# Performance work log

Hardware: AMD Instinct MI355X
Metric: run time of the kernel (lower is better)

## Reference

```python
import jax, jax.numpy as jnp
import numpy as np

N_NODES = 20000


def _gcn_norm(edge_index, n):
    src, dst = edge_index[0], edge_index[1]
    # degree of A + I (self-loops), all edge weights 1
    deg = jax.ops.segment_sum(jnp.ones(src.shape[0], jnp.float32), dst, num_segments=n) + 1.0
    dinv = jax.lax.rsqrt(deg)
    norm = dinv[src] * dinv[dst]          # [E]
    self_norm = dinv * dinv               # [N] self-loop coefficient = 1/deg
    return src, dst, norm, self_norm


def _gcn_layer(x, W, b, src, dst, norm, self_norm):
    # x: [B, N, Fin]; W: [Fin, Fout]
    h = jnp.einsum('bnf,fo->bno', x, W)   # transform first (PyG GCNConv order)
    msg = h[:, src, :] * norm[None, :, None]                      # [B, E, Fout]
    agg = jax.vmap(lambda m: jax.ops.segment_sum(m, dst, num_segments=x.shape[1]))(msg)
    agg = agg + h * self_norm[None, :, None]                      # self-loop term
    return agg + b


def setup_inputs() -> dict:
    key = jax.random.key(0)
    ks = jax.random.split(key, 8)
    B, N, Fin, H, O, E = 2, N_NODES, 256, 256, 64, 320000
    s = lambda f: 1.0 / np.sqrt(f)
    return {
        'x': jax.random.normal(ks[0], (B, N, Fin), jnp.float32),
        'W1': jax.random.normal(ks[1], (Fin, H), jnp.float32) * s(Fin),
        'b1': jnp.zeros((H,), jnp.float32),
        'W2': jax.random.normal(ks[2], (H, H), jnp.float32) * s(H),
        'b2': jnp.zeros((H,), jnp.float32),
        'Wfc': jax.random.normal(ks[3], (H, O), jnp.float32) * s(H),
        'bfc': jnp.zeros((O,), jnp.float32),
        'edge_index': jax.random.randint(ks[4], (2, E), 0, N, jnp.int64),
    }


def reference(x, W1, b1, W2, b2, Wfc, bfc, edge_index):
    src, dst, norm, self_norm = _gcn_norm(edge_index, x.shape[1])
    h = jax.nn.relu(_gcn_layer(x, W1, b1, src, dst, norm, self_norm))
    h = jax.nn.relu(_gcn_layer(h, W2, b2, src, dst, norm, self_norm))
    pooled = jnp.mean(h, axis=1)          # mean over nodes -> [B, H]
    return pooled @ Wfc + bfc             # [B, O]
```

## Files before the change

### kernel.cpp

```cpp
#include <hip/hip_runtime.h>

#define NNODES 20000
#define BATCH  2
#define FEAT   256
#define OOUT   64
#define PBLK   200
#define MROWS  (BATCH * NNODES)
#define MPAD   40192

typedef short  bhalf8 __attribute__((ext_vector_type(8)));
typedef float  floatx4 __attribute__((ext_vector_type(4)));
typedef float  floatx2 __attribute__((ext_vector_type(2)));

__device__ __forceinline__ float bf2f(unsigned short u) {
  return __uint_as_float(((unsigned int)u) << 16);
}
__device__ __forceinline__ unsigned short f2bf(float f) {
  unsigned int u = __float_as_uint(f);
  return (unsigned short)((u + 0x7fffu + ((u >> 16) & 1u)) >> 16);
}

__device__ __forceinline__ unsigned int pack4_fp8(float a, float b, float c, float d) {
  int p = __builtin_amdgcn_cvt_pk_fp8_f32(a, b, 0, false);
  p = __builtin_amdgcn_cvt_pk_fp8_f32(c, d, p, true);
  return (unsigned int)p;
}

__global__ __launch_bounds__(256) void detect_zero_kernel(const int* __restrict__ raw,
                                                          int* __restrict__ flag,
                                                          int* __restrict__ cnt,
                                                          int* __restrict__ fill, int E) {
  for (int i = threadIdx.x; i < NNODES; i += 256) { cnt[i] = 0; fill[i] = 0; }
  __shared__ int any;
  if (threadIdx.x == 0) any = 0;
  __syncthreads();
  int nchk = E < 2048 ? E : 2048;
  for (int i = threadIdx.x; i < nchk; i += blockDim.x)
    if (raw[2 * i + 1] != 0) any = 1;
  __syncthreads();
  if (threadIdx.x == 0) *flag = any;
}

__global__ void convert_count_kernel(const int* __restrict__ raw, const int* __restrict__ flag,
                                     int* __restrict__ s32, int* __restrict__ d32,
                                     int* __restrict__ cnt, int E) {
  int e = blockIdx.x * blockDim.x + threadIdx.x;
  if (e >= E) return;
  int s, d;
  if (*flag) { s = raw[e];     d = raw[E + e]; }
  else       { s = raw[2 * e]; d = raw[2 * (E + e)]; }
  s32[e] = s; d32[e] = d;
  atomicAdd(&cnt[d], 1);
}

__global__ __launch_bounds__(1024) void scan_dinv_kernel(const int* __restrict__ cnt,
                                                         int* __restrict__ row_start,
                                                         float* __restrict__ dinv, int n) {
  __shared__ int wsum[16];
  __shared__ int carry_s;
  int tid = threadIdx.x, lane = tid & 63, wv = tid >> 6;
  if (tid == 0) carry_s = 0;
  __syncthreads();
  for (int base = 0; base < n; base += 1024) {
    int v = (base + tid < n) ? cnt[base + tid] : 0;
    if (base + tid < n) dinv[base + tid] = 1.0f / sqrtf((float)(v + 1));
    int x = v;
#pragma unroll
    for (int off = 1; off < 64; off <<= 1) {
      int t = __shfl_up(x, off);
      if (lane >= off) x += t;
    }
    if (lane == 63) wsum[wv] = x;
    __syncthreads();
    int carry = carry_s;
    if (wv == 0) {
      int s = (lane < 16) ? wsum[lane] : 0;
#pragma unroll
      for (int off = 1; off < 16; off <<= 1) {
        int t = __shfl_up(s, off);
        if (lane >= off) s += t;
      }
      if (lane < 16) wsum[lane] = s;
    }
    __syncthreads();
    int woff = wv ? wsum[wv - 1] : 0;
    int total = wsum[15];
    if (base + tid < n) row_start[base + tid] = carry + woff + x - v;
    __syncthreads();
    if (tid == 0) carry_s = carry + total;
  }
  if (tid == 0) row_start[n] = carry_s;
}

__global__ void scatter_kernel(const int* __restrict__ s32, const int* __restrict__ d32,
                               const int* __restrict__ row_start, int* __restrict__ fill,
                               const float* __restrict__ dinv,
                               int* __restrict__ csr_src, float* __restrict__ csr_norm, int E) {
  int e = blockIdx.x * blockDim.x + threadIdx.x;
  if (e >= E) return;
  int s = s32[e], d = d32[e];
  int p = row_start[d] + atomicAdd(&fill[d], 1);
  csr_src[p] = s;
  csr_norm[p] = dinv[s] * dinv[d];
}

__global__ __launch_bounds__(256) void wprep_kernel(const float* __restrict__ W1,
                                                    const float* __restrict__ W2,
                                                    unsigned short* __restrict__ W1hi,
                                                    unsigned short* __restrict__ W1lo,
                                                    unsigned short* __restrict__ W2hi,
                                                    unsigned short* __restrict__ W2lo) {
  int which = blockIdx.x >> 8;
  int idx = (blockIdx.x & 255) * 256 + threadIdx.x;
  const float* W = which ? W2 : W1;
  unsigned short* Whi = which ? W2hi : W1hi;
  unsigned short* Wlo = which ? W2lo : W1lo;
  int k = idx >> 8, n = idx & 255;
  float w = W[idx];
  unsigned short hi = f2bf(w);
  unsigned short lo = f2bf(w - bf2f(hi));
  int g = n >> 4, ln = n & 15;
  int ks = k >> 5, ch = (k >> 3) & 3, j = k & 7;
  int addr = ((ks * 16 + g) * 64 + ch * 16 + ln) * 8 + j;
  Whi[addr] = hi;
  Wlo[addr] = lo;
}

template <int AFP32>
__global__ __launch_bounds__(256) void gemm_mfma(const void* __restrict__ Av,
                                                 const unsigned short* __restrict__ Whi,
                                                 const unsigned short* __restrict__ Wlo,
                                                 unsigned int* __restrict__ C) {
  __shared__ unsigned short lds[2][8192];
  int tid = threadIdx.x, lane = tid & 63, wv = tid >> 6;
  int half = blockIdx.y;
  int bm = blockIdx.x * 128;
  int kc = (lane >> 4) * 8;

  const float* Af          = (const float*)Av;
  const unsigned short* Ab = (const unsigned short*)Av;

  int mr[2];
#pragma unroll
  for (int t = 0; t < 2; ++t) {
    int m = bm + wv * 32 + t * 16 + (lane & 15);
    mr[t] = m >= MROWS ? MROWS - 1 : m;
  }

  floatx4 acc[2][8];
#pragma unroll
  for (int t = 0; t < 2; ++t)
#pragma unroll
    for (int g = 0; g < 8; ++g) acc[t][g] = (floatx4)(0.0f);

  bhalf8 st[4];

  auto stage_load = [&](int ks) {
#pragma unroll
    for (int i2 = 0; i2 < 4; ++i2) {
      int u = i2 * 256 + tid;
      int hl = u >> 9, g = (u >> 6) & 7, l = u & 63;
      const unsigned short* Wp = hl ? Wlo : Whi;
      st[i2] = *(const bhalf8*)&Wp[((size_t)(ks * 16 + half * 8 + g) * 64 + l) * 8];
    }
  };
  auto stage_write = [&](int buf) {
#pragma unroll
    for (int i2 = 0; i2 < 4; ++i2) {
      int u = i2 * 256 + tid;
      *(bhalf8*)&lds[buf][(size_t)u * 8] = st[i2];
    }
  };
  auto load_a = [&](int ks, bhalf8 (&a)[2]) {
#pragma unroll
    for (int t = 0; t < 2; ++t) {
      if (AFP32) {
        const float* p = &Af[(size_t)mr[t] * FEAT + ks * 32 + kc];
        float4 u = *(const float4*)p;
        float4 v = *(const float4*)(p + 4);
        a[t][0] = (short)f2bf(u.x); a[t][1] = (short)f2bf(u.y);
        a[t][2] = (short)f2bf(u.z); a[t][3] = (short)f2bf(u.w);
        a[t][4] = (short)f2bf(v.x); a[t][5] = (short)f2bf(v.y);
        a[t][6] = (short)f2bf(v.z); a[t][7] = (short)f2bf(v.w);
      } else {
        a[t] = *(const bhalf8*)&Ab[(size_t)mr[t] * FEAT + ks * 32 + kc];
      }
    }
  };
  auto step = [&](int buf, bhalf8 (&a)[2]) {
#pragma unroll
    for (int g = 0; g < 8; ++g) {
      bhalf8 bh = *(const bhalf8*)&lds[buf][((size_t)g * 64 + lane) * 8];
      bhalf8 bl = *(const bhalf8*)&lds[buf][((size_t)(512 + g * 64) + lane) * 8];
#pragma unroll
      for (int t = 0; t < 2; ++t)
        acc[t][g] = __builtin_amdgcn_mfma_f32_16x16x32_bf16(bh, a[t], acc[t][g], 0, 0, 0);
#pragma unroll
      for (int t = 0; t < 2; ++t)
        acc[t][g] = __builtin_amdgcn_mfma_f32_16x16x32_bf16(bl, a[t], acc[t][g], 0, 0, 0);
    }
  };

  stage_load(0);
  stage_write(0);
  __syncthreads();
  bhalf8 aC[2];
  load_a(0, aC);
  int cur = 0;
#pragma unroll
  for (int ks = 0; ks < 8; ++ks) {
    bhalf8 aN[2];
    if (ks < 7) {
      stage_load(ks + 1);
      load_a(ks + 1, aN);
    }
    step(cur, aC);
    if (ks < 7) {
      stage_write(cur ^ 1);
      __syncthreads();
      aC[0] = aN[0]; aC[1] = aN[1];
    }
    cur ^= 1;
  }

  int nc = (lane >> 4) * 4;
#pragma unroll
  for (int t = 0; t < 2; ++t) {
    int om = bm + wv * 32 + t * 16 + (lane & 15);
#pragma unroll
    for (int g = 0; g < 8; ++g) {
      int col = (half * 8 + g) * 16 + nc;
      C[(size_t)om * 64 + (col >> 2)] =
          pack4_fp8(acc[t][g][0], acc[t][g][1], acc[t][g][2], acc[t][g][3]);
    }
  }
}

__global__ __launch_bounds__(128) void agg_kernel(const uint4* __restrict__ h8,
                                                  const int* __restrict__ row_start,
                                                  const int* __restrict__ csr_src,
                                                  const float* __restrict__ csr_norm,
                                                  const float* __restrict__ dinv,
                                                  const float* __restrict__ bias,
                                                  unsigned short* __restrict__ out) {
  int n = blockIdx.x;
  int b = threadIdx.x >> 6;
  int lane = threadIdx.x & 63;
  int q = lane >> 4;
  int cl = lane & 15;
  const uint4* hb = h8 + (size_t)b * NNODES * 16;

  float a[16];
#pragma unroll
  for (int j = 0; j < 16; ++j) a[j] = 0.0f;

  auto dec_fma = [&](uint4 m, float w) {
    unsigned int mm[4] = {m.x, m.y, m.z, m.w};
#pragma unroll
    for (int j = 0; j < 4; ++j) {
      floatx2 lo = __builtin_amdgcn_cvt_pk_f32_fp8((int)mm[j], false);
      floatx2 hi = __builtin_amdgcn_cvt_pk_f32_fp8((int)mm[j], true);
      a[j * 4 + 0] = fmaf(w, lo[0], a[j * 4 + 0]);
      a[j * 4 + 1] = fmaf(w, lo[1], a[j * 4 + 1]);
      a[j * 4 + 2] = fmaf(w, hi[0], a[j * 4 + 2]);
      a[j * 4 + 3] = fmaf(w, hi[1], a[j * 4 + 3]);
    }
  };

  float di = dinv[n];
  if (q == 0) dec_fma(hb[(size_t)n * 16 + cl], di * di);

  int s0 = row_start[n], s1 = row_start[n + 1];
  int i = s0 + q;
  for (; i + 4 < s1; i += 8) {
    int sa = csr_src[i], sb = csr_src[i + 4];
    float wa = csr_norm[i], wb = csr_norm[i + 4];
    uint4 ma = hb[(size_t)sa * 16 + cl];
    uint4 mb = hb[(size_t)sb * 16 + cl];
    dec_fma(ma, wa);
    dec_fma(mb, wb);
  }
  if (i < s1) dec_fma(hb[(size_t)csr_src[i] * 16 + cl], csr_norm[i]);

#pragma unroll
  for (int j = 0; j < 16; ++j) {
    a[j] += __shfl_xor(a[j], 16);
    a[j] += __shfl_xor(a[j], 32);
  }

  if (q == 0) {
    int c = cl * 16;
    unsigned short o[16];
#pragma unroll
    for (int j = 0; j < 16; ++j)
      o[j] = f2bf(fmaxf(a[j] + bias[c + j], 0.0f));
    unsigned short* dst = &out[((size_t)b * NNODES + n) * FEAT + c];
    *(uint4*)dst = *(uint4*)&o[0];
    *(uint4*)(dst + 8) = *(uint4*)&o[8];
  }
}

__global__ __launch_bounds__(256) void pool_partial(const unsigned short* __restrict__ h2,
                                                    float* __restrict__ partials) {
  int blk = blockIdx.x;
  int c = threadIdx.x;
  int chunk = NNODES / PBLK;
  int n0 = blk * chunk;
  float s0 = 0.f, s1 = 0.f;
  for (int n = n0; n < n0 + chunk; ++n) {
    s0 += bf2f(h2[((size_t)0 * NNODES + n) * FEAT + c]);
    s1 += bf2f(h2[((size_t)1 * NNODES + n) * FEAT + c]);
  }
  partials[(blk * 2 + 0) * FEAT + c] = s0;
  partials[(blk * 2 + 1) * FEAT + c] = s1;
}

__global__ __launch_bounds__(256) void pool_fc(const float* __restrict__ partials,
                                               const float* __restrict__ Wfc, const float* __restrict__ bfc,
                                               float* __restrict__ out) {
  __shared__ float pooled[BATCH][FEAT];
  int t = threadIdx.x;
  float s0 = 0.f, s1 = 0.f;
  for (int p = 0; p < PBLK; ++p) {
    s0 += partials[(p * 2 + 0) * FEAT + t];
    s1 += partials[(p * 2 + 1) * FEAT + t];
  }
  pooled[0][t] = s0 / (float)NNODES;
  pooled[1][t] = s1 / (float)NNODES;
  __syncthreads();
  if (t < BATCH * OOUT) {
    int b = t >> 6, o = t & 63;
    float acc = bfc[o];
    for (int c2 = 0; c2 < FEAT; ++c2)
      acc = fmaf(pooled[b][c2], Wfc[c2 * OOUT + o], acc);
    out[b * OOUT + o] = acc;
  }
}

extern "C" void kernel_launch(void* const* d_in, const int* in_sizes, int n_in,
                              void* d_out, int out_size, void* d_ws, size_t ws_size,
                              hipStream_t stream) {
  const float* x    = (const float*)d_in[0];
  const float* W1   = (const float*)d_in[1];
  const float* b1   = (const float*)d_in[2];
  const float* W2   = (const float*)d_in[3];
  const float* b2   = (const float*)d_in[4];
  const float* Wfc  = (const float*)d_in[5];
  const float* bfc  = (const float*)d_in[6];
  const int*   eraw = (const int*)d_in[7];
  int E = in_sizes[7] / 2;
  float* out = (float*)d_out;

  char* ws = (char*)d_ws;
  size_t off = 0;
  auto alloc = [&](size_t elems) -> void* {
    void* p = ws + off * 4;
    off += (elems + 3) & ~(size_t)3;
    return p;
  };
  int*   flag      = (int*)alloc(4);
  int*   s32       = (int*)alloc(E);
  int*   d32      = (int*)alloc(E);
  int*   cnt       = (int*)alloc(NNODES);
  float* dinv      = (float*)alloc(NNODES);
  int*   row_start = (int*)alloc(NNODES + 1);
  int*   fill      = (int*)alloc(NNODES);
  int*   csr_src   = (int*)alloc(E);
  float* csr_norm  = (float*)alloc(E);
  unsigned short* w1hi = (unsigned short*)alloc(65536 / 2);
  unsigned short* w1lo = (unsigned short*)alloc(65536 / 2);
  unsigned short* w2hi = (unsigned short*)alloc(65536 / 2);
  unsigned short* w2lo = (unsigned short*)alloc(65536 / 2);
  unsigned int*   h8   = (unsigned int*)alloc((size_t)MPAD * 64);
  unsigned short* a1   = (unsigned short*)alloc((size_t)MROWS * FEAT / 2);
  float* partials  = (float*)alloc((size_t)PBLK * BATCH * FEAT);

  int eg = (E + 255) / 256;
  detect_zero_kernel<<<1, 256, 0, stream>>>(eraw, flag, cnt, fill, E);
  convert_count_kernel<<<eg, 256, 0, stream>>>(eraw, flag, s32, d32, cnt, E);
  scan_dinv_kernel<<<1, 1024, 0, stream>>>(cnt, row_start, dinv, NNODES);
  scatter_kernel<<<eg, 256, 0, stream>>>(s32, d32, row_start, fill, dinv, csr_src, csr_norm, E);
  wprep_kernel<<<512, 256, 0, stream>>>(W1, W2, w1hi, w1lo, w2hi, w2lo);

  dim3 ggrid(MPAD / 128, 2);
  gemm_mfma<1><<<ggrid, 256, 0, stream>>>(x, w1hi, w1lo, h8);
  agg_kernel<<<NNODES, 128, 0, stream>>>((const uint4*)h8, row_start, csr_src, csr_norm, dinv, b1, a1);
  gemm_mfma<0><<<ggrid, 256, 0, stream>>>(a1, w2hi, w2lo, h8);
  agg_kernel<<<NNODES, 128, 0, stream>>>((const uint4*)h8, row_start, csr_src, csr_norm, dinv, b2, a1);
  pool_partial<<<PBLK, 256, 0, stream>>>(a1, partials);
  pool_fc<<<1, 256, 0, stream>>>(partials, Wfc, bfc, out);
}
```

Before: 203.0 us.

## Fuse all GCN stages into one cooperative persistent megakernel with grid syncs

Replaces the chain of separate launches (CSR build, weight prep, two GEMMs, two aggregations, pooling, FC) with a single cooperative kernel that walks through the stages using grid-wide barriers. It also fuses the second aggregation with mean-pooling so the second-layer activations are never written out, and parallelizes the degree scan across blocks. The goal is to remove launch gaps and one full activation round trip, at the cost of grid-sync overhead, a fixed persistent grid that may underfill some stages, and register pressure from the merged code.

Measured after the change: 695.7 us. +242.7%, slower.

```diff
diff --git a/kernel.cpp b/kernel.cpp
--- a/kernel.cpp
+++ b/kernel.cpp
@@ -1,12 +1,16 @@
 #include <hip/hip_runtime.h>
+#include <hip/hip_cooperative_groups.h>
+
+namespace cg = cooperative_groups;
 
 #define NNODES 20000
 #define BATCH  2
 #define FEAT   256
 #define OOUT   64
-#define PBLK   200
-#define MROWS  (BATCH * NNODES)
+#define MROWS  40000
 #define MPAD   40192
+#define NTILES 628
+#define NCHUNK 20
 
 typedef short  bhalf8 __attribute__((ext_vector_type(8)));
 typedef float  floatx4 __attribute__((ext_vector_type(4)));
@@ -19,124 +23,29 @@
   unsigned int u = __float_as_uint(f);
   return (unsigned short)((u + 0x7fffu + ((u >> 16) & 1u)) >> 16);
 }
-
 __device__ __forceinline__ unsigned int pack4_fp8(float a, float b, float c, float d) {
   int p = __builtin_amdgcn_cvt_pk_fp8_f32(a, b, 0, false);
   p = __builtin_amdgcn_cvt_pk_fp8_f32(c, d, p, true);
   return (unsigned int)p;
 }
 
-__global__ __launch_bounds__(256) void detect_zero_kernel(const int* __restrict__ raw,
-                                                          int* __restrict__ flag,
-                                                          int* __restrict__ cnt,
-                                                          int* __restrict__ fill, int E) {
-  for (int i = threadIdx.x; i < NNODES; i += 256) { cnt[i] = 0; fill[i] = 0; }
-  __shared__ int any;
-  if (threadIdx.x == 0) any = 0;
-  __syncthreads();
-  int nchk = E < 2048 ? E : 2048;
-  for (int i = threadIdx.x; i < nchk; i += blockDim.x)
-    if (raw[2 * i + 1] != 0) any = 1;
-  __syncthreads();
-  if (threadIdx.x == 0) *flag = any;
-}
-
-__global__ void convert_count_kernel(const int* __restrict__ raw, const int* __restrict__ flag,
-                                     int* __restrict__ s32, int* __restrict__ d32,
-                                     int* __restrict__ cnt, int E) {
-  int e = blockIdx.x * blockDim.x + threadIdx.x;
-  if (e >= E) return;
-  int s, d;
-  if (*flag) { s = raw[e];     d = raw[E + e]; }
-  else       { s = raw[2 * e]; d = raw[2 * (E + e)]; }
-  s32[e] = s; d32[e] = d;
-  atomicAdd(&cnt[d], 1);
-}
-
-__global__ __launch_bounds__(1024) void scan_dinv_kernel(const int* __restrict__ cnt,
-                                                         int* __restrict__ row_start,
-                                                         float* __restrict__ dinv, int n) {
-  __shared__ int wsum[16];
-  __shared__ int carry_s;
+struct GArgs {
+  const float *x, *W1, *b1, *W2, *b2, *Wfc, *bfc;
+  const int* eraw;
+  int E;
+  int *flag, *s32, *d32, *cnt, *row_start, *fill, *csr_src, *chunkAux;
+  float *dinv, *csr_norm, *partials, *out;
+  unsigned short *w1hi, *w1lo, *w2hi, *w2lo, *a1;
+  unsigned int* h8;
+};
+
+template <int AFP32>
+__device__ __forceinline__ void gemm_tile(const void* Av, const unsigned short* Whi,
+                                          const unsigned short* Wlo, unsigned int* C,
+                                          int bx, int half, unsigned short* ldsb) {
   int tid = threadIdx.x, lane = tid & 63, wv = tid >> 6;
-  if (tid == 0) carry_s = 0;
-  __syncthreads();
-  for (int base = 0; base < n; base += 1024) {
-    int v = (base + tid < n) ? cnt[base + tid] : 0;
-    if (base + tid < n) dinv[base + tid] = 1.0f / sqrtf((float)(v + 1));
-    int x = v;
-#pragma unroll
-    for (int off = 1; off < 64; off <<= 1) {
-      int t = __shfl_up(x, off);
-      if (lane >= off) x += t;
-    }
-    if (lane == 63) wsum[wv] = x;
-    __syncthreads();
-    int carry = carry_s;
-    if (wv == 0) {
-      int s = (lane < 16) ? wsum[lane] : 0;
-#pragma unroll
-      for (int off = 1; off < 16; off <<= 1) {
-        int t = __shfl_up(s, off);
-        if (lane >= off) s += t;
-      }
-      if (lane < 16) wsum[lane] = s;
-    }
-    __syncthreads();
-    int woff = wv ? wsum[wv - 1] : 0;
-    int total = wsum[15];
-    if (base + tid < n) row_start[base + tid] = carry + woff + x - v;
-    __syncthreads();
-    if (tid == 0) carry_s = carry + total;
-  }
-  if (tid == 0) row_start[n] = carry_s;
-}
-
-__global__ void scatter_kernel(const int* __restrict__ s32, const int* __restrict__ d32,
-                               const int* __restrict__ row_start, int* __restrict__ fill,
-                               const float* __restrict__ dinv,
-                               int* __restrict__ csr_src, float* __restrict__ csr_norm, int E) {
-  int e = blockIdx.x * blockDim.x + threadIdx.x;
-  if (e >= E) return;
-  int s = s32[e], d = d32[e];
-  int p = row_start[d] + atomicAdd(&fill[d], 1);
-  csr_src[p] = s;
-  csr_norm[p] = dinv[s] * dinv[d];
-}
-
-__global__ __launch_bounds__(256) void wprep_kernel(const float* __restrict__ W1,
-                                                    const float* __restrict__ W2,
-                                                    unsigned short* __restrict__ W1hi,
-                                                    unsigned short* __restrict__ W1lo,
-                                                    unsigned short* __restrict__ W2hi,
-                                                    unsigned short* __restrict__ W2lo) {
-  int which = blockIdx.x >> 8;
-  int idx = (blockIdx.x & 255) * 256 + threadIdx.x;
-  const float* W = which ? W2 : W1;
-  unsigned short* Whi = which ? W2hi : W1hi;
-  unsigned short* Wlo = which ? W2lo : W1lo;
-  int k = idx >> 8, n = idx & 255;
-  float w = W[idx];
-  unsigned short hi = f2bf(w);
-  unsigned short lo = f2bf(w - bf2f(hi));
-  int g = n >> 4, ln = n & 15;
-  int ks = k >> 5, ch = (k >> 3) & 3, j = k & 7;
-  int addr = ((ks * 16 + g) * 64 + ch * 16 + ln) * 8 + j;
-  Whi[addr] = hi;
-  Wlo[addr] = lo;
-}
-
-template <int AFP32>
-__global__ __launch_bounds__(256) void gemm_mfma(const void* __restrict__ Av,
-                                                 const unsigned short* __restrict__ Whi,
-                                                 const unsigned short* __restrict__ Wlo,
-                                                 unsigned int* __restrict__ C) {
-  __shared__ unsigned short lds[2][8192];
-  int tid = threadIdx.x, lane = tid & 63, wv = tid >> 6;
-  int half = blockIdx.y;
-  int bm = blockIdx.x * 128;
+  int bm = bx * 128;
   int kc = (lane >> 4) * 8;
-
   const float* Af          = (const float*)Av;
   const unsigned short* Ab = (const unsigned short*)Av;
 
@@ -146,7 +55,6 @@
     int m = bm + wv * 32 + t * 16 + (lane & 15);
     mr[t] = m >= MROWS ? MROWS - 1 : m;
   }
-
   floatx4 acc[2][8];
 #pragma unroll
   for (int t = 0; t < 2; ++t)
@@ -154,7 +62,6 @@
     for (int g = 0; g < 8; ++g) acc[t][g] = (floatx4)(0.0f);
 
   bhalf8 st[4];
-
   auto stage_load = [&](int ks) {
 #pragma unroll
     for (int i2 = 0; i2 < 4; ++i2) {
@@ -168,7 +75,7 @@
 #pragma unroll
     for (int i2 = 0; i2 < 4; ++i2) {
       int u = i2 * 256 + tid;
-      *(bhalf8*)&lds[buf][(size_t)u * 8] = st[i2];
+      *(bhalf8*)&ldsb[(size_t)buf * 8192 + (size_t)u * 8] = st[i2];
     }
   };
   auto load_a = [&](int ks, bhalf8 (&a)[2]) {
@@ -190,8 +97,8 @@
   auto step = [&](int buf, bhalf8 (&a)[2]) {
 #pragma unroll
     for (int g = 0; g < 8; ++g) {
-      bhalf8 bh = *(const bhalf8*)&lds[buf][((size_t)g * 64 + lane) * 8];
-      bhalf8 bl = *(const bhalf8*)&lds[buf][((size_t)(512 + g * 64) + lane) * 8];
+      bhalf8 bh = *(const bhalf8*)&ldsb[(size_t)buf * 8192 + ((size_t)g * 64 + lane) * 8];
+      bhalf8 bl = *(const bhalf8*)&ldsb[(size_t)buf * 8192 + ((size_t)(512 + g * 64) + lane) * 8];
 #pragma unroll
       for (int t = 0; t < 2; ++t)
         acc[t][g] = __builtin_amdgcn_mfma_f32_16x16x32_bf16(bh, a[t], acc[t][g], 0, 0, 0);
@@ -236,19 +143,14 @@
   }
 }
 
-__global__ __launch_bounds__(128) void agg_kernel(const uint4* __restrict__ h8,
-                                                  const int* __restrict__ row_start,
-                                                  const int* __restrict__ csr_src,
-                                                  const float* __restrict__ csr_norm,
-                                                  const float* __restrict__ dinv,
-                                                  const float* __restrict__ bias,
-                                                  unsigned short* __restrict__ out) {
-  int n = blockIdx.x;
-  int b = threadIdx.x >> 6;
-  int lane = threadIdx.x & 63;
+template <int WRITE>
+__device__ __forceinline__ void agg_node(const GArgs& g, int n, int tid2,
+                                         const float* bias, float* pacc) {
+  int b = tid2 >> 6;
+  int lane = tid2 & 63;
   int q = lane >> 4;
   int cl = lane & 15;
-  const uint4* hb = h8 + (size_t)b * NNODES * 16;
+  const uint4* hb = (const uint4*)g.h8 + (size_t)b * NNODES * 16;
 
   float a[16];
 #pragma unroll
@@ -267,20 +169,20 @@
     }
   };
 
-  float di = dinv[n];
+  float di = g.dinv[n];
   if (q == 0) dec_fma(hb[(size_t)n * 16 + cl], di * di);
 
-  int s0 = row_start[n], s1 = row_start[n + 1];
+  int s0 = g.row_start[n], s1 = g.row_start[n + 1];
   int i = s0 + q;
   for (; i + 4 < s1; i += 8) {
-    int sa = csr_src[i], sb = csr_src[i + 4];
-    float wa = csr_norm[i], wb = csr_norm[i + 4];
+    int sa = g.csr_src[i], sb = g.csr_src[i + 4];
+    float wa = g.csr_norm[i], wb = g.csr_norm[i + 4];
     uint4 ma = hb[(size_t)sa * 16 + cl];
     uint4 mb = hb[(size_t)sb * 16 + cl];
     dec_fma(ma, wa);
     dec_fma(mb, wb);
   }
-  if (i < s1) dec_fma(hb[(size_t)csr_src[i] * 16 + cl], csr_norm[i]);
+  if (i < s1) dec_fma(hb[(size_t)g.csr_src[i] * 16 + cl], g.csr_norm[i]);
 
 #pragma unroll
   for (int j = 0; j < 16; ++j) {
@@ -288,105 +190,220 @@
     a[j] += __shfl_xor(a[j], 32);
   }
 
-  if (q == 0) {
-    int c = cl * 16;
-    unsigned short o[16];
-#pragma unroll
-    for (int j = 0; j < 16; ++j)
-      o[j] = f2bf(fmaxf(a[j] + bias[c + j], 0.0f));
-    unsigned short* dst = &out[((size_t)b * NNODES + n) * FEAT + c];
-    *(uint4*)dst = *(uint4*)&o[0];
-    *(uint4*)(dst + 8) = *(uint4*)&o[8];
-  }
-}
-
-__global__ __launch_bounds__(256) void pool_partial(const unsigned short* __restrict__ h2,
-                                                    float* __restrict__ partials) {
-  int blk = blockIdx.x;
-  int c = threadIdx.x;
-  int chunk = NNODES / PBLK;
-  int n0 = blk * chunk;
-  float s0 = 0.f, s1 = 0.f;
-  for (int n = n0; n < n0 + chunk; ++n) {
-    s0 += bf2f(h2[((size_t)0 * NNODES + n) * FEAT + c]);
-    s1 += bf2f(h2[((size_t)1 * NNODES + n) * FEAT + c]);
-  }
-  partials[(blk * 2 + 0) * FEAT + c] = s0;
-  partials[(blk * 2 + 1) * FEAT + c] = s1;
-}
-
-__global__ __launch_bounds__(256) void pool_fc(const float* __restrict__ partials,
-                                               const float* __restrict__ Wfc, const float* __restrict__ bfc,
-                                               float* __restrict__ out) {
-  __shared__ float pooled[BATCH][FEAT];
-  int t = threadIdx.x;
-  float s0 = 0.f, s1 = 0.f;
-  for (int p = 0; p < PBLK; ++p) {
-    s0 += partials[(p * 2 + 0) * FEAT + t];
-    s1 += partials[(p * 2 + 1) * FEAT + t];
-  }
-  pooled[0][t] = s0 / (float)NNODES;
-  pooled[1][t] = s1 / (float)NNODES;
-  __syncthreads();
-  if (t < BATCH * OOUT) {
-    int b = t >> 6, o = t & 63;
-    float acc = bfc[o];
-    for (int c2 = 0; c2 < FEAT; ++c2)
-      acc = fmaf(pooled[b][c2], Wfc[c2 * OOUT + o], acc);
-    out[b * OOUT + o] = acc;
+  if (WRITE) {
+    if (q == 0) {
+      int c = cl * 16;
+      unsigned short o[16];
+#pragma unroll
+      for (int j = 0; j < 16; ++j)
+        o[j] = f2bf(fmaxf(a[j] + bias[c + j], 0.0f));
+      unsigned short* dst = &g.a1[((size_t)b * NNODES + n) * FEAT + c];
+      *(uint4*)dst = *(uint4*)&o[0];
+      *(uint4*)(dst + 8) = *(uint4*)&o[8];
+    }
+  } else {
+    if (q == 0) {
+      int c = cl * 16;
+#pragma unroll
+      for (int j = 0; j < 16; ++j)
+        pacc[j] += fmaxf(a[j] + bias[c + j], 0.0f);
+    }
+  }
+}
+
+__global__ __launch_bounds__(256) void GCN_mega(GArgs g) {
+  cg::grid_group gg = cg::this_grid();
+  __shared__ __align__(16) char smem[32768];
+  const int tid = threadIdx.x, bid = blockIdx.x;
+  const int nblk = (int)gridDim.x;
+  const int nthr = nblk * 256;
+  const int gtid = bid * 256 + tid;
+
+  for (int i = gtid; i < NNODES; i += nthr) { g.cnt[i] = 0; g.fill[i] = 0; }
+  for (int idx = gtid; idx < 2 * FEAT * FEAT; idx += nthr) {
+    int which = idx >> 16, loc = idx & 65535;
+    const float* W = which ? g.W2 : g.W1;
+    unsigned short* Whi = which ? g.w2hi : g.w1hi;
+    unsigned short* Wlo = which ? g.w2lo : g.w1lo;
+    int k = loc >> 8, n = loc & 255;
+    float w = W[loc];
+    unsigned short hi = f2bf(w);
+    unsigned short lo = f2bf(w - bf2f(hi));
+    int gq = n >> 4, ln = n & 15;
+    int ks = k >> 5, ch = (k >> 3) & 3, j = k & 7;
+    int addr = ((ks * 16 + gq) * 64 + ch * 16 + ln) * 8 + j;
+    Whi[addr] = hi;
+    Wlo[addr] = lo;
+  }
+  if (bid == 0) {
+    int* any = (int*)smem;
+    if (tid == 0) *any = 0;
+    __syncthreads();
+    int nchk = g.E < 2048 ? g.E : 2048;
+    for (int i = tid; i < nchk; i += 256)
+      if (g.eraw[2 * i + 1] != 0) *any = 1;
+    __syncthreads();
+    if (tid == 0) *g.flag = *any;
+  }
+  gg.sync();
+
+  {
+    int isI32 = *g.flag;
+    for (int e = gtid; e < g.E; e += nthr) {
+      int s, d;
+      if (isI32) { s = g.eraw[e];     d = g.eraw[g.E + e]; }
+      else       { s = g.eraw[2 * e]; d = g.eraw[2 * (g.E + e)]; }
+      g.s32[e] = s; g.d32[e] = d;
+      atomicAdd(&g.cnt[d], 1);
+    }
+  }
+  gg.sync();
+
+  if (bid < NCHUNK) {
+    int base = bid * 1024 + tid * 4;
+    int v[4]; int tsum = 0;
+#pragma unroll
+    for (int j = 0; j < 4; ++j) { v[j] = (base + j < NNODES) ? g.cnt[base + j] : 0; tsum += v[j]; }
+    int lane = tid & 63, wv = tid >> 6;
+    int x = tsum;
+#pragma unroll
+    for (int off = 1; off < 64; off <<= 1) { int t = __shfl_up(x, off); if (lane >= off) x += t; }
+    int* wsum = (int*)smem;
+    if (lane == 63) wsum[wv] = x;
+    __syncthreads();
+    int woff = 0;
+    for (int w = 0; w < wv; ++w) woff += wsum[w];
+    int run = woff + x - tsum;
+#pragma unroll
+    for (int j = 0; j < 4; ++j) {
+      if (base + j < NNODES) {
+        g.row_start[base + j] = run;
+        g.dinv[base + j] = 1.0f / sqrtf((float)(v[j] + 1));
+      }
+      run += v[j];
+    }
+    if (tid == 0) g.chunkAux[bid] = wsum[0] + wsum[1] + wsum[2] + wsum[3];
+  }
+  gg.sync();
+
+  if (bid == 0 && tid == 0) {
+    int tot = 0;
+    for (int c = 0; c < NCHUNK; ++c) { int t = g.chunkAux[c]; g.chunkAux[c] = tot; tot += t; }
+    g.row_start[NNODES] = tot;
+  }
+  gg.sync();
+
+  for (int i = gtid; i < NNODES; i += nthr) g.row_start[i] += g.chunkAux[i >> 10];
+  gg.sync();
+
+  for (int e = gtid; e < g.E; e += nthr) {
+    int s = g.s32[e], d = g.d32[e];
+    int p = g.row_start[d] + atomicAdd(&g.fill[d], 1);
+    g.csr_src[p] = s;
+    g.csr_norm[p] = g.dinv[s] * g.dinv[d];
+  }
+  gg.sync();
+
+  for (int t = bid; t < NTILES; t += nblk)
+    gemm_tile<1>(g.x, g.w1hi, g.w1lo, g.h8, t >> 1, t & 1, (unsigned short*)smem);
+  gg.sync();
+
+  {
+    int nsub = tid >> 7, tid2 = tid & 127;
+    for (int n = bid * 2 + nsub; n < NNODES; n += nblk * 2)
+      agg_node<1>(g, n, tid2, g.b1, (float*)nullptr);
+  }
+  gg.sync();
+
+  for (int t = bid; t < NTILES; t += nblk)
+    gemm_tile<0>(g.a1, g.w2hi, g.w2lo, g.h8, t >> 1, t & 1, (unsigned short*)smem);
+  gg.sync();
+
+  {
+    float pacc[16];
+#pragma unroll
+    for (int j = 0; j < 16; ++j) pacc[j] = 0.0f;
+    int nsub = tid >> 7, tid2 = tid & 127;
+    for (int n = bid * 2 + nsub; n < NNODES; n += nblk * 2)
+      agg_node<0>(g, n, tid2, g.b2, pacc);
+
+    float* sp = (float*)smem;
+    for (int t2 = tid; t2 < 512; t2 += 256) sp[t2] = 0.0f;
+    __syncthreads();
+    int b = tid2 >> 6, lane = tid2 & 63, q = lane >> 4, cl = lane & 15;
+    if (q == 0) {
+#pragma unroll
+      for (int j = 0; j < 16; ++j)
+        atomicAdd(&sp[b * 256 + cl * 16 + j], pacc[j]);
+    }
+    __syncthreads();
+    for (int t2 = tid; t2 < 512; t2 += 256)
+      g.partials[(size_t)bid * 512 + t2] = sp[t2];
+  }
+  gg.sync();
+
+  if (bid < 2) {
+    float* pooled = (float*)smem;
+    float s = 0.0f;
+    for (int p = 0; p < nblk; ++p) s += g.partials[(size_t)p * 512 + bid * 256 + tid];
+    pooled[tid] = s / (float)NNODES;
+    __syncthreads();
+    if (tid < OOUT) {
+      float acc = g.bfc[tid];
+      for (int f = 0; f < FEAT; ++f)
+        acc = fmaf(pooled[f], g.Wfc[f * OOUT + tid], acc);
+      g.out[bid * OOUT + tid] = acc;
+    }
   }
 }
 
 extern "C" void kernel_launch(void* const* d_in, const int* in_sizes, int n_in,
                               void* d_out, int out_size, void* d_ws, size_t ws_size,
                               hipStream_t stream) {
-  const float* x    = (const float*)d_in[0];
-  const float* W1   = (const float*)d_in[1];
-  const float* b1   = (const float*)d_in[2];
-  const float* W2   = (const float*)d_in[3];
-  const float* b2   = (const float*)d_in[4];
-  const float* Wfc  = (const float*)d_in[5];
-  const float* bfc  = (const float*)d_in[6];
-  const int*   eraw = (const int*)d_in[7];
-  int E = in_sizes[7] / 2;
-  float* out = (float*)d_out;
+  GArgs a;
+  a.x    = (const float*)d_in[0];
+  a.W1   = (const float*)d_in[1];
+  a.b1   = (const float*)d_in[2];
+  a.W2   = (const float*)d_in[3];
+  a.b2   = (const float*)d_in[4];
+  a.Wfc  = (const float*)d_in[5];
+  a.bfc  = (const float*)d_in[6];
+  a.eraw = (const int*)d_in[7];
+  a.E    = in_sizes[7] / 2;
+  a.out  = (float*)d_out;
 
   char* ws = (char*)d_ws;
   size_t off = 0;
-  auto alloc = [&](size_t elems) -> void* {
+  auto alloc = [&](size_t elems4B) -> void* {
     void* p = ws + off * 4;
-    off += (elems + 3) & ~(size_t)3;
+    off += (elems4B + 3) & ~(size_t)3;
     return p;
   };
-  int*   flag      = (int*)alloc(4);
-  int*   s32       = (int*)alloc(E);
-  int*   d32      = (int*)alloc(E);
-  int*   cnt       = (int*)alloc(NNODES);
-  float* dinv      = (float*)alloc(NNODES);
-  int*   row_start = (int*)alloc(NNODES + 1);
-  int*   fill      = (int*)alloc(NNODES);
-  int*   csr_src   = (int*)alloc(E);
-  float* csr_norm  = (float*)alloc(E);
-  unsigned short* w1hi = (unsigned short*)alloc(65536 / 2);
-  unsigned short* w1lo = (unsigned short*)alloc(65536 / 2);
-  unsigned short* w2hi = (unsigned short*)alloc(65536 / 2);
-  unsigned short* w2lo = (unsigned short*)alloc(65536 / 2);
-  unsigned int*   h8   = (unsigned int*)alloc((size_t)MPAD * 64);
-  unsigned short* a1   = (unsigned short*)alloc((size_t)MROWS * FEAT / 2);
-  float* partials  = (float*)alloc((size_t)PBLK * BATCH * FEAT);
-
-  int eg = (E + 255) / 256;
-  detect_zero_kernel<<<1, 256, 0, stream>>>(eraw, flag, cnt, fill, E);
-  convert_count_kernel<<<eg, 256, 0, stream>>>(eraw, flag, s32, d32, cnt, E);
-  scan_dinv_kernel<<<1, 1024, 0, stream>>>(cnt, row_start, dinv, NNODES);
-  scatter_kernel<<<eg, 256, 0, stream>>>(s32, d32, row_start, fill, dinv, csr_src, csr_norm, E);
-  wprep_kernel<<<512, 256, 0, stream>>>(W1, W2, w1hi, w1lo, w2hi, w2lo);
-
-  dim3 ggrid(MPAD / 128, 2);
-  gemm_mfma<1><<<ggrid, 256, 0, stream>>>(x, w1hi, w1lo, h8);
-  agg_kernel<<<NNODES, 128, 0, stream>>>((const uint4*)h8, row_start, csr_src, csr_norm, dinv, b1, a1);
-  gemm_mfma<0><<<ggrid, 256, 0, stream>>>(a1, w2hi, w2lo, h8);
-  agg_kernel<<<NNODES, 128, 0, stream>>>((const uint4*)h8, row_start, csr_src, csr_norm, dinv, b2, a1);
-  pool_partial<<<PBLK, 256, 0, stream>>>(a1, partials);
-  pool_fc<<<1, 256, 0, stream>>>(partials, Wfc, bfc, out);
-}
+  int E = a.E;
+  a.flag      = (int*)alloc(4);
+  a.s32       = (int*)alloc(E);
+  a.d32       = (int*)alloc(E);
+  a.cnt       = (int*)alloc(NNODES);
+  a.dinv      = (float*)alloc(NNODES);
+  a.row_start = (int*)alloc(NNODES + 1);
+  a.fill      = (int*)alloc(NNODES);
+  a.csr_src   = (int*)alloc(E);
+  a.csr_norm  = (float*)alloc(E);
+  a.chunkAux  = (int*)alloc(32);
+  a.w1hi = (unsigned short*)alloc(65536 / 2);
+  a.w1lo = (unsigned short*)alloc(65536 / 2);
+  a.w2hi = (unsigned short*)alloc(65536 / 2);
+  a.w2lo = (unsigned short*)alloc(65536 / 2);
+  a.h8   = (unsigned int*)alloc((size_t)MPAD * 64);
+  a.a1   = (unsigned short*)alloc((size_t)MROWS * FEAT / 2);
+  a.partials = (float*)alloc((size_t)1024 * 512);
+
+  int nb = 0;
+  hipOccupancyMaxActiveBlocksPerMultiprocessor(&nb, GCN_mega, 256, 0);
+  if (nb < 1) nb = 1;
+  int grid = nb * 256;
+  if (grid > 1024) grid = 1024;
+
+  void* kp[1] = {&a};
+  hipLaunchCooperativeKernel(GCN_mega, dim3(grid), dim3(256), kp, 0, stream);
+}
```

## Interleave batch rows in fp8 features so one gather serves both batches

Applied to the files above, without the earlier changes.

The GEMM now writes the fp8 transformed features with the two batch copies of each node stored next to each other (row = node*2 + batch). Each neighbour gather in aggregation then fetches one contiguous 512-byte row covering both batches, instead of two separate 256-byte rows. The aggregation is re-split so each wave half handles different edges across all 32 column chunks, with an LDS step to combine the two waves. Weight prep, counter zeroing and the edge-format check are also merged into a single prep kernel to cut launches.

Result: faster. 188.9 us (-6.9%).

```diff
diff --git a/kernel.cpp b/kernel.cpp
--- a/kernel.cpp
+++ b/kernel.cpp
@@ -5,8 +5,9 @@
 #define FEAT   256
 #define OOUT   64
 #define PBLK   200
-#define MROWS  (BATCH * NNODES)
-#define MPAD   40192
+#define MROWS  40000
+#define NPB    20096
+#define H8ROWS 40192
 
 typedef short  bhalf8 __attribute__((ext_vector_type(8)));
 typedef float  floatx4 __attribute__((ext_vector_type(4)));
@@ -19,26 +20,48 @@
   unsigned int u = __float_as_uint(f);
   return (unsigned short)((u + 0x7fffu + ((u >> 16) & 1u)) >> 16);
 }
-
 __device__ __forceinline__ unsigned int pack4_fp8(float a, float b, float c, float d) {
   int p = __builtin_amdgcn_cvt_pk_fp8_f32(a, b, 0, false);
   p = __builtin_amdgcn_cvt_pk_fp8_f32(c, d, p, true);
   return (unsigned int)p;
 }
 
-__global__ __launch_bounds__(256) void detect_zero_kernel(const int* __restrict__ raw,
-                                                          int* __restrict__ flag,
-                                                          int* __restrict__ cnt,
-                                                          int* __restrict__ fill, int E) {
-  for (int i = threadIdx.x; i < NNODES; i += 256) { cnt[i] = 0; fill[i] = 0; }
-  __shared__ int any;
-  if (threadIdx.x == 0) any = 0;
-  __syncthreads();
-  int nchk = E < 2048 ? E : 2048;
-  for (int i = threadIdx.x; i < nchk; i += blockDim.x)
-    if (raw[2 * i + 1] != 0) any = 1;
-  __syncthreads();
-  if (threadIdx.x == 0) *flag = any;
+__global__ __launch_bounds__(256) void prep_kernel(const float* __restrict__ W1,
+                                                   const float* __restrict__ W2,
+                                                   unsigned short* __restrict__ w1hi,
+                                                   unsigned short* __restrict__ w1lo,
+                                                   unsigned short* __restrict__ w2hi,
+                                                   unsigned short* __restrict__ w2lo,
+                                                   const int* __restrict__ raw, int E,
+                                                   int* __restrict__ flag,
+                                                   int* __restrict__ cnt,
+                                                   int* __restrict__ fill) {
+  int bid = blockIdx.x, tid = threadIdx.x;
+  int idx = bid * 256 + tid;
+  int which = idx >> 16, loc = idx & 65535;
+  const float* W = which ? W2 : W1;
+  unsigned short* Whi = which ? w2hi : w1hi;
+  unsigned short* Wlo = which ? w2lo : w1lo;
+  int k = loc >> 8, n = loc & 255;
+  float w = W[loc];
+  unsigned short hi = f2bf(w);
+  unsigned short lo = f2bf(w - bf2f(hi));
+  int g = n >> 4, ln = n & 15;
+  int ks = k >> 5, ch = (k >> 3) & 3, j = k & 7;
+  int addr = ((ks * 16 + g) * 64 + ch * 16 + ln) * 8 + j;
+  Whi[addr] = hi;
+  Wlo[addr] = lo;
+  if (idx < NNODES) { cnt[idx] = 0; fill[idx] = 0; }
+  if (bid == 511) {
+    __shared__ int any;
+    if (tid == 0) any = 0;
+    __syncthreads();
+    int nchk = E < 2048 ? E : 2048;
+    for (int i = tid; i < nchk; i += 256)
+      if (raw[2 * i + 1] != 0) any = 1;
+    __syncthreads();
+    if (tid == 0) *flag = any;
+  }
 }
 
 __global__ void convert_count_kernel(const int* __restrict__ raw, const int* __restrict__ flag,
@@ -104,47 +127,29 @@
   csr_norm[p] = dinv[s] * dinv[d];
 }
 
-__global__ __launch_bounds__(256) void wprep_kernel(const float* __restrict__ W1,
-                                                    const float* __restrict__ W2,
-                                                    unsigned short* __restrict__ W1hi,
-                                                    unsigned short* __restrict__ W1lo,
-                                                    unsigned short* __restrict__ W2hi,
-                                                    unsigned short* __restrict__ W2lo) {
-  int which = blockIdx.x >> 8;
-  int idx = (blockIdx.x & 255) * 256 + threadIdx.x;
-  const float* W = which ? W2 : W1;
-  unsigned short* Whi = which ? W2hi : W1hi;
-  unsigned short* Wlo = which ? W2lo : W1lo;
-  int k = idx >> 8, n = idx & 255;
-  float w = W[idx];
-  unsigned short hi = f2bf(w);
-  unsigned short lo = f2bf(w - bf2f(hi));
-  int g = n >> 4, ln = n & 15;
-  int ks = k >> 5, ch = (k >> 3) & 3, j = k & 7;
-  int addr = ((ks * 16 + g) * 64 + ch * 16 + ln) * 8 + j;
-  Whi[addr] = hi;
-  Wlo[addr] = lo;
-}
-
 template <int AFP32>
 __global__ __launch_bounds__(256) void gemm_mfma(const void* __restrict__ Av,
                                                  const unsigned short* __restrict__ Whi,
                                                  const unsigned short* __restrict__ Wlo,
                                                  unsigned int* __restrict__ C) {
   __shared__ unsigned short lds[2][8192];
+  int bid = blockIdx.x;
+  int tile = bid >> 1, half = bid & 1;
+  int b = tile >= 157 ? 1 : 0;
+  int nbase = (tile - b * 157) * 128;
   int tid = threadIdx.x, lane = tid & 63, wv = tid >> 6;
-  int half = blockIdx.y;
-  int bm = blockIdx.x * 128;
   int kc = (lane >> 4) * 8;
 
   const float* Af          = (const float*)Av;
   const unsigned short* Ab = (const unsigned short*)Av;
 
-  int mr[2];
+  int nn[2], mr[2];
 #pragma unroll
   for (int t = 0; t < 2; ++t) {
-    int m = bm + wv * 32 + t * 16 + (lane & 15);
-    mr[t] = m >= MROWS ? MROWS - 1 : m;
+    int nl = nbase + wv * 32 + t * 16 + (lane & 15);
+    nn[t] = nl;
+    int ncl = nl > NNODES - 1 ? NNODES - 1 : nl;
+    mr[t] = b * NNODES + ncl;
   }
 
   floatx4 acc[2][8];
@@ -154,7 +159,6 @@
     for (int g = 0; g < 8; ++g) acc[t][g] = (floatx4)(0.0f);
 
   bhalf8 st[4];
-
   auto stage_load = [&](int ks) {
 #pragma unroll
     for (int i2 = 0; i2 < 4; ++i2) {
@@ -226,11 +230,11 @@
   int nc = (lane >> 4) * 4;
 #pragma unroll
   for (int t = 0; t < 2; ++t) {
-    int om = bm + wv * 32 + t * 16 + (lane & 15);
+    size_t r = (size_t)nn[t] * 2 + b;
 #pragma unroll
     for (int g = 0; g < 8; ++g) {
       int col = (half * 8 + g) * 16 + nc;
-      C[(size_t)om * 64 + (col >> 2)] =
+      C[r * 64 + (col >> 2)] =
           pack4_fp8(acc[t][g][0], acc[t][g][1], acc[t][g][2], acc[t][g][3]);
     }
   }
@@ -244,11 +248,10 @@
                                                   const float* __restrict__ bias,
                                                   unsigned short* __restrict__ out) {
   int n = blockIdx.x;
-  int b = threadIdx.x >> 6;
-  int lane = threadIdx.x & 63;
-  int q = lane >> 4;
-  int cl = lane & 15;
-  const uint4* hb = h8 + (size_t)b * NNODES * 16;
+  int tid = threadIdx.x;
+  int wave = tid >> 6, lane = tid & 63;
+  int q = (wave << 1) | (lane >> 5);
+  int cl = lane & 31;
 
   float a[16];
 #pragma unroll
@@ -268,28 +271,34 @@
   };
 
   float di = dinv[n];
-  if (q == 0) dec_fma(hb[(size_t)n * 16 + cl], di * di);
+  if (q == 0) dec_fma(h8[(size_t)n * 32 + cl], di * di);
 
   int s0 = row_start[n], s1 = row_start[n + 1];
   int i = s0 + q;
   for (; i + 4 < s1; i += 8) {
     int sa = csr_src[i], sb = csr_src[i + 4];
     float wa = csr_norm[i], wb = csr_norm[i + 4];
-    uint4 ma = hb[(size_t)sa * 16 + cl];
-    uint4 mb = hb[(size_t)sb * 16 + cl];
+    uint4 ma = h8[(size_t)sa * 32 + cl];
+    uint4 mb = h8[(size_t)sb * 32 + cl];
     dec_fma(ma, wa);
     dec_fma(mb, wb);
   }
-  if (i < s1) dec_fma(hb[(size_t)csr_src[i] * 16 + cl], csr_norm[i]);
-
-#pragma unroll
-  for (int j = 0; j < 16; ++j) {
-    a[j] += __shfl_xor(a[j], 16);
-    a[j] += __shfl_xor(a[j], 32);
-  }
-
-  if (q == 0) {
-    int c = cl * 16;
+  if (i < s1) dec_fma(h8[(size_t)csr_src[i] * 32 + cl], csr_norm[i]);
+
+#pragma unroll
+  for (int j = 0; j < 16; ++j) a[j] += __shfl_xor(a[j], 32);
+
+  __shared__ float red[32][17];
+  if (wave == 1 && lane < 32) {
+#pragma unroll
+    for (int j = 0; j < 16; ++j) red[lane][j] = a[j];
+  }
+  __syncthreads();
+  if (wave == 0 && lane < 32) {
+    int b = cl >> 4;
+    int c = (cl & 15) * 16;
+#pragma unroll
+    for (int j = 0; j < 16; ++j) a[j] += red[lane][j];
     unsigned short o[16];
 #pragma unroll
     for (int j = 0; j < 16; ++j)
@@ -353,14 +362,14 @@
 
   char* ws = (char*)d_ws;
   size_t off = 0;
-  auto alloc = [&](size_t elems) -> void* {
+  auto alloc = [&](size_t elems4B) -> void* {
     void* p = ws + off * 4;
-    off += (elems + 3) & ~(size_t)3;
+    off += (elems4B + 3) & ~(size_t)3;
     return p;
   };
   int*   flag      = (int*)alloc(4);
   int*   s32       = (int*)alloc(E);
-  int*   d32      = (int*)alloc(E);
+  int*   d32       = (int*)alloc(E);
   int*   cnt       = (int*)alloc(NNODES);
   float* dinv      = (float*)alloc(NNODES);
   int*   row_start = (int*)alloc(NNODES + 1);
@@ -371,21 +380,19 @@
   unsigned short* w1lo = (unsigned short*)alloc(65536 / 2);
   unsigned short* w2hi = (unsigned short*)alloc(65536 / 2);
   unsigned short* w2lo = (unsigned short*)alloc(65536 / 2);
-  unsigned int*   h8   = (unsigned int*)alloc((size_t)MPAD * 64);
+  unsigned int*   h8   = (unsigned int*)alloc((size_t)H8ROWS * 64);
   unsigned short* a1   = (unsigned short*)alloc((size_t)MROWS * FEAT / 2);
   float* partials  = (float*)alloc((size_t)PBLK * BATCH * FEAT);
 
   int eg = (E + 255) / 256;
-  detect_zero_kernel<<<1, 256, 0, stream>>>(eraw, flag, cnt, fill, E);
+  prep_kernel<<<512, 256, 0, stream>>>(W1, W2, w1hi, w1lo, w2hi, w2lo, eraw, E, flag, cnt, fill);
   convert_count_kernel<<<eg, 256, 0, stream>>>(eraw, flag, s32, d32, cnt, E);
   scan_dinv_kernel<<<1, 1024, 0, stream>>>(cnt, row_start, dinv, NNODES);
   scatter_kernel<<<eg, 256, 0, stream>>>(s32, d32, row_start, fill, dinv, csr_src, csr_norm, E);
-  wprep_kernel<<<512, 256, 0, stream>>>(W1, W2, w1hi, w1lo, w2hi, w2lo);
-
-  dim3 ggrid(MPAD / 128, 2);
-  gemm_mfma<1><<<ggrid, 256, 0, stream>>>(x, w1hi, w1lo, h8);
+
+  gemm_mfma<1><<<628, 256, 0, stream>>>(x, w1hi, w1lo, h8);
   agg_kernel<<<NNODES, 128, 0, stream>>>((const uint4*)h8, row_start, csr_src, csr_norm, dinv, b1, a1);
-  gemm_mfma<0><<<ggrid, 256, 0, stream>>>(a1, w2hi, w2lo, h8);
+  gemm_mfma<0><<<628, 256, 0, stream>>>(a1, w2hi, w2lo, h8);
   agg_kernel<<<NNODES, 128, 0, stream>>>((const uint4*)h8, row_start, csr_src, csr_norm, dinv, b2, a1);
   pool_partial<<<PBLK, 256, 0, stream>>>(a1, partials);
   pool_fc<<<1, 256, 0, stream>>>(partials, Wfc, bfc, out);
```
